# Optimization experiments

Hardware: AMD Instinct MI355X
Metric: run time of the kernel (lower is better)

Reference implementation:

```python
import jax, jax.numpy as jnp
import numpy as np

B, P, IN_DIM, OUT_DIM = 4, 120000, 4, 64
SPATIAL = (480, 360, 32)
EPS = 1e-5
SLOPE = 0.01  # LeakyReLU default negative slope


def setup_inputs() -> dict:
    key = jax.random.key(0)
    ks = jax.random.split(key, 10)
    pc = jax.random.normal(ks[0], (B, P, IN_DIM), dtype=jnp.float32)
    pc_indices = jax.random.randint(ks[1], (B, P, 3), 0, 32, dtype=jnp.int32)
    W1 = jax.random.normal(ks[2], (IN_DIM, 16), dtype=jnp.float32) * (1.0 / np.sqrt(IN_DIM))
    b1 = jax.random.normal(ks[3], (16,), dtype=jnp.float32) * 0.01
    g1 = jnp.ones((16,), jnp.float32)
    be1 = jnp.zeros((16,), jnp.float32)
    W2 = jax.random.normal(ks[4], (16, OUT_DIM), dtype=jnp.float32) * 0.25
    b2 = jax.random.normal(ks[5], (OUT_DIM,), dtype=jnp.float32) * 0.01
    g2 = jnp.ones((OUT_DIM,), jnp.float32)
    be2 = jnp.zeros((OUT_DIM,), jnp.float32)
    return {"pc": pc, "pc_indices": pc_indices, "W1": W1, "b1": b1, "g1": g1,
            "be1": be1, "W2": W2, "b2": b2, "g2": g2, "be2": be2}


def _bn_lrelu(h, g, b):
    # BatchNorm1d in training mode: batch mean / biased variance over points
    mean = jnp.mean(h, axis=0)
    var = jnp.mean((h - mean) ** 2, axis=0)
    h = (h - mean) / jnp.sqrt(var + EPS) * g + b
    return jnp.where(h >= 0, h, SLOPE * h)


def reference(pc, pc_indices, W1, b1, g1, be1, W2, b2, g2, be2):
    N = B * P
    x = pc.reshape(N, IN_DIM)
    bid = jnp.repeat(jnp.arange(B, dtype=jnp.int32), P)  # batch id padded in front
    coords = jnp.concatenate([bid[:, None], pc_indices.reshape(N, 3)], axis=1)  # [N,4]

    # small MLP (shuffle/recover in the original is a mathematical no-op for outputs)
    h = _bn_lrelu(x @ W1 + b1, g1, be1)
    feat = _bn_lrelu(h @ W2 + b2, g2, be2)  # [N, OUT_DIM]

    # torch.unique(dim=0) == lexicographic sort of linearized voxel keys
    S0, S1, S2 = SPATIAL
    key = (((coords[:, 0] * S0 + coords[:, 1]) * S1 + coords[:, 2]) * S2 + coords[:, 3])
    order = jnp.argsort(key)
    sk = key[order]
    is_first = jnp.concatenate([jnp.ones((1,), bool), sk[1:] != sk[:-1]])
    seg_sorted = (jnp.cumsum(is_first) - 1).astype(jnp.int32)  # segment id per sorted point
    inv = jnp.zeros((N,), jnp.int32).at[order].set(seg_sorted)  # inverse index (unsorted)

    # scatter_max into (padded, fixed-shape) voxel feature table
    voxel_feat = jax.ops.segment_max(feat, inv, num_segments=N)  # [N, OUT_DIM]
    n_uni = seg_sorted[-1] + 1
    valid = jnp.arange(N) < n_uni
    voxel_feat = jnp.where(valid[:, None], voxel_feat, 0.0)
    voxel_ind = jnp.zeros((N, 4), jnp.int32).at[seg_sorted].set(coords[order])

    return voxel_feat, voxel_ind, feat
```

## Files before the change

### kernel.cpp

```cpp
#include <hip/hip_runtime.h>

typedef unsigned int u32;
typedef unsigned long long u64;

#define N_PTS 480000
#define PPB   120000
#define NKEY  131072
#define NBLK_A 256
#define NBLK_B 256
#define SLOPE 0.01f

__global__ __launch_bounds__(256) void kA0(const float* __restrict__ pc,
                                           const int* __restrict__ pidx,
                                           u32* __restrict__ keys,
                                           u32* __restrict__ cnt,
                                           float* __restrict__ pA) {
    int t = threadIdx.x;
    int g = blockIdx.x * 256 + t;
    ((u64*)cnt)[g] = 0ull;

    float a[14];
#pragma unroll
    for (int j = 0; j < 14; ++j) a[j] = 0.f;

    for (int n = g; n < N_PTS; n += NBLK_A * 256) {
        float4 x = ((const float4*)pc)[n];
        a[0] += x.x; a[1] += x.y; a[2] += x.z; a[3] += x.w;
        a[4] += x.x * x.x; a[5] += x.x * x.y; a[6]  += x.x * x.z; a[7]  += x.x * x.w;
        a[8] += x.y * x.y; a[9] += x.y * x.z; a[10] += x.y * x.w;
        a[11] += x.z * x.z; a[12] += x.z * x.w; a[13] += x.w * x.w;

        int i0 = pidx[3 * n], i1 = pidx[3 * n + 1], i2 = pidx[3 * n + 2];
        int bid = n / PPB;
        keys[n] = (u32)(bid * 32768 + i0 * 1024 + i1 * 32 + i2);
    }

    __shared__ float red[256];
    for (int j = 0; j < 14; ++j) {
        red[t] = a[j];
        __syncthreads();
        for (int s = 128; s > 0; s >>= 1) {
            if (t < s) red[t] += red[t + s];
            __syncthreads();
        }
        if (t == 0) pA[j * NBLK_A + blockIdx.x] = red[0];
        __syncthreads();
    }
}

__global__ __launch_bounds__(256, 1) void kB(const float* __restrict__ pc,
                                             const u32* __restrict__ keys,
                                             const float* __restrict__ pA,
                                             const float* __restrict__ W1,
                                             const float* __restrict__ b1,
                                             const float* __restrict__ g1,
                                             const float* __restrict__ be1,
                                             u32* __restrict__ cnt,
                                             float* __restrict__ pB,
                                             float* __restrict__ stats1) {
    int t = threadIdx.x, w = t >> 6, lane = t & 63;
    __shared__ float S[14];
    __shared__ float sW[80];
    __shared__ float sred[4][152];

    for (int q = w; q < 14; q += 4) {
        const float* p = pA + q * NBLK_A;
        float s = p[lane] + p[lane + 64] + p[lane + 128] + p[lane + 192];
        for (int d = 32; d > 0; d >>= 1) s += __shfl_xor(s, d);
        if (lane == 0) S[q] = s;
    }
    __syncthreads();
    if (t < 16) {
        int c = t;
        double w4[4];
#pragma unroll
        for (int i = 0; i < 4; ++i) w4[i] = W1[i * 16 + c];
        double sx[4] = { S[0], S[1], S[2], S[3] };
        auto sxx = [&](int i, int j) -> double {
            if (i > j) { int k = i; i = j; j = k; }
            int base = (i == 0) ? 4 : (i == 1) ? 8 : (i == 2) ? 11 : 13;
            return (double)S[base + (j - i)];
        };
        double su = 0.0;
        for (int i = 0; i < 4; ++i) su += sx[i] * w4[i];
        double q = 0.0;
        for (int i = 0; i < 4; ++i)
            for (int j = 0; j < 4; ++j) q += w4[i] * w4[j] * sxx(i, j);
        double b = (double)b1[c];
        double sum   = su + b * (double)N_PTS;
        double sumsq = q + 2.0 * b * su + (double)N_PTS * b * b;
        double mean = sum / (double)N_PTS;
        double var  = sumsq / (double)N_PTS - mean * mean;
        float inv = rsqrtf((float)(var + 1e-5));
        float sc = g1[c] * inv;
        float sf = be1[c] - (float)mean * sc;
#pragma unroll
        for (int i = 0; i < 4; ++i) sW[c * 4 + i] = W1[i * 16 + c] * sc;
        sW[64 + c] = b1[c] * sc + sf;
        if (blockIdx.x == 0) {
#pragma unroll
            for (int i = 0; i < 4; ++i) stats1[c * 4 + i] = sW[c * 4 + i];
            stats1[64 + c] = sW[64 + c];
        }
    }
    __syncthreads();

    for (int n = blockIdx.x * 256 + t; n < N_PTS; n += NBLK_B * 256)
        atomicAdd(&cnt[keys[n]], 1u);

    float acc[152];
#pragma unroll
    for (int m = 0; m < 152; ++m) acc[m] = 0.f;

    const float4* sW4 = (const float4*)sW;
    for (int n = blockIdx.x * 256 + t; n < N_PTS; n += NBLK_B * 256) {
        float4 x = ((const float4*)pc)[n];
        float h[16];
#pragma unroll
        for (int k = 0; k < 16; ++k) {
            float4 wk = sW4[k];
            float z = x.x * wk.x + x.y * wk.y + x.z * wk.z + x.w * wk.w + sW[64 + k];
            h[k] = (z >= 0.f) ? z : SLOPE * z;
        }
#pragma unroll
        for (int i = 0; i < 16; ++i) acc[i] += h[i];
#pragma unroll
        for (int i = 0; i < 16; ++i)
#pragma unroll
            for (int j = i; j < 16; ++j)
                acc[16 + i * 16 - (i * (i - 1)) / 2 + (j - i)] += h[i] * h[j];
    }

#pragma unroll
    for (int m = 0; m < 152; ++m) {
        float s = acc[m];
        for (int d = 32; d > 0; d >>= 1) s += __shfl_xor(s, d);
        acc[m] = s;
    }
    if (lane == 0) {
#pragma unroll
        for (int m = 0; m < 152; ++m) sred[w][m] = acc[m];
    }
    __syncthreads();
    if (t < 152)
        pB[t * NBLK_B + blockIdx.x] = sred[0][t] + sred[1][t] + sred[2][t] + sred[3][t];
}

__global__ __launch_bounds__(256) void kS1(const u32* __restrict__ cnt,
                                           u32* __restrict__ bsum,
                                           const float* __restrict__ pB,
                                           const float* __restrict__ W2,
                                           const float* __restrict__ b2,
                                           const float* __restrict__ g2,
                                           const float* __restrict__ be2,
                                           float* __restrict__ stats2) {
    int t = threadIdx.x, b = blockIdx.x;
    uint4 c4 = ((const uint4*)cnt)[b * 256 + t];
    u32 cs = c4.x + c4.y + c4.z + c4.w;
    u32 os = (c4.x > 0) + (c4.y > 0) + (c4.z > 0) + (c4.w > 0);
    __shared__ u32 rc[256], ro[256];
    rc[t] = cs; ro[t] = os;
    __syncthreads();
    for (int s = 128; s > 0; s >>= 1) {
        if (t < s) { rc[t] += rc[t + s]; ro[t] += ro[t + s]; }
        __syncthreads();
    }
    if (t == 0) { bsum[2 * b] = rc[0]; bsum[2 * b + 1] = ro[0]; }

    if (b == 0) {
        int w = t >> 6, lane = t & 63;
        __shared__ float S[152];
        for (int q = w; q < 152; q += 4) {
            const float* p = pB + q * NBLK_B;
            float s = p[lane] + p[lane + 64] + p[lane + 128] + p[lane + 192];
            for (int d = 32; d > 0; d >>= 1) s += __shfl_xor(s, d);
            if (lane == 0) S[q] = s;
        }
        __syncthreads();
        if (t < 64) {
            double wv[16];
#pragma unroll
            for (int k = 0; k < 16; ++k) wv[k] = W2[k * 64 + t];
            double sh = 0.0;
            for (int k = 0; k < 16; ++k) sh += wv[k] * (double)S[k];
            auto qidx = [&](int i, int j) { return 16 + i * 16 - (i * (i - 1)) / 2 + (j - i); };
            double q = 0.0;
            for (int i = 0; i < 16; ++i) {
                q += wv[i] * wv[i] * (double)S[qidx(i, i)];
                double t2 = 0.0;
                for (int j = i + 1; j < 16; ++j) t2 += wv[j] * (double)S[qidx(i, j)];
                q += 2.0 * wv[i] * t2;
            }
            double bb = (double)b2[t];
            double sum   = sh + bb * (double)N_PTS;
            double sumsq = q + 2.0 * bb * sh + (double)N_PTS * bb * bb;
            double mean = sum / (double)N_PTS;
            double var  = sumsq / (double)N_PTS - mean * mean;
            float inv = rsqrtf((float)(var + 1e-5));
            float scs = g2[t] * inv;
            float sf = be2[t] - (float)mean * scs;
#pragma unroll
            for (int k = 0; k < 16; ++k) stats2[k * 64 + t] = W2[k * 64 + t] * scs;
            stats2[1024 + t] = b2[t] * scs + sf;
        }
    }
}

__global__ __launch_bounds__(256) void kS2(u32* __restrict__ cnt,
                                           const u32* __restrict__ bsum,
                                           u32* __restrict__ startc,
                                           float* __restrict__ vi,
                                           u32* __restrict__ nuni) {
    int t = threadIdx.x, b = blockIdx.x;
    __shared__ u32 sbc[128], sbo[128];
    __shared__ u32 cOff, oOff;
    __shared__ u64 scan[256];
    if (t < 128) { sbc[t] = bsum[2 * t]; sbo[t] = bsum[2 * t + 1]; }

    uint4 c4 = ((const uint4*)cnt)[b * 256 + t];
    u32 cv[4] = { c4.x, c4.y, c4.z, c4.w };
    u32 cs = cv[0] + cv[1] + cv[2] + cv[3];
    u32 os = (cv[0] > 0) + (cv[1] > 0) + (cv[2] > 0) + (cv[3] > 0);
    scan[t] = ((u64)cs << 32) | (u64)os;
    __syncthreads();
    if (t == 0) {
        u32 a = 0, o = 0;
        for (int i = 0; i < b; ++i) { a += sbc[i]; o += sbo[i]; }
        cOff = a; oOff = o;
    }
    for (int d = 1; d < 256; d <<= 1) {
        u64 v = (t >= d) ? scan[t - d] : 0ull;
        __syncthreads();
        scan[t] += v;
        __syncthreads();
    }
    u64 ex = scan[t] - (((u64)cs << 32) | (u64)os);
    u32 start = cOff + (u32)(ex >> 32);
    u32 rank  = oOff + (u32)(ex & 0xffffffffull);

    int kbase = b * 1024 + t * 4;
#pragma unroll
    for (int j = 0; j < 4; ++j) {
        u32 k = (u32)(kbase + j);
        cnt[k] = start;
        if (cv[j] > 0) {
            startc[rank] = start;
            float4 o;
            o.x = (float)(k >> 15);
            o.y = (float)((k >> 10) & 31);
            o.z = (float)((k >> 5) & 31);
            o.w = (float)(k & 31);
            ((float4*)vi)[rank] = o;
            rank++;
        }
        start += cv[j];
    }
    if (b == 127 && t == 255) {
        nuni[0] = rank;
        startc[rank] = N_PTS;
    }
}

__global__ __launch_bounds__(256) void kP(const u32* __restrict__ keys,
                                          u32* __restrict__ cursor,
                                          u32* __restrict__ pid) {
    int n = blockIdx.x * 256 + threadIdx.x;
    if (n < N_PTS) {
        u32 k = keys[n];
        u32 pos = atomicAdd(&cursor[k], 1u);
        pid[pos] = (u32)n;
    }
}

__global__ __launch_bounds__(256) void kW(const float* __restrict__ pc,
                                          const u32* __restrict__ pid,
                                          const u32* __restrict__ startc,
                                          const u32* __restrict__ nuni,
                                          const float* __restrict__ stats1,
                                          const float* __restrict__ stats2,
                                          float* __restrict__ feat,
                                          float* __restrict__ vf,
                                          float* __restrict__ vi) {
    u32 nu = *nuni;
    int w = threadIdx.x >> 6, lane = threadIdx.x & 63;

    int k1 = lane & 15;
    float w1c[4];
#pragma unroll
    for (int i = 0; i < 4; ++i) w1c[i] = stats1[k1 * 4 + i];
    float c1 = stats1[64 + k1];

    float w2c[16];
#pragma unroll
    for (int k = 0; k < 16; ++k) w2c[k] = stats2[k * 64 + lane];
    float c2f = stats2[1024 + lane];

    for (u32 r = blockIdx.x * 4 + (u32)w; r < N_PTS; r += 8192) {
        if (r < nu) {
            u32 s = startc[r], e = startc[r + 1];
            float m = -3.4e38f;
            for (u32 i = s; i < e; ++i) {
                u32 p = pid[i];
                float4 x = ((const float4*)pc)[p];
                float hk = x.x * w1c[0] + x.y * w1c[1] + x.z * w1c[2] + x.w * w1c[3] + c1;
                hk = (hk >= 0.f) ? hk : SLOPE * hk;
                u32 hbits = __float_as_uint(hk);
                float f = c2f;
#pragma unroll
                for (int k = 0; k < 16; ++k) {
                    float hv = __uint_as_float((u32)__builtin_amdgcn_readlane((int)hbits, k));
                    f += hv * w2c[k];
                }
                f = (f >= 0.f) ? f : SLOPE * f;
                feat[(size_t)p * 64 + lane] = f;
                m = fmaxf(m, f);
            }
            vf[(size_t)r * 64 + lane] = m;
        } else {
            vf[(size_t)r * 64 + lane] = 0.f;
            if (lane < 4) vi[(size_t)r * 4 + lane] = 0.f;
        }
    }
}

extern "C" void kernel_launch(void* const* d_in, const int* in_sizes, int n_in,
                              void* d_out, int out_size, void* d_ws, size_t ws_size,
                              hipStream_t stream) {
    const float* pc   = (const float*)d_in[0];
    const int*   pidx = (const int*)d_in[1];
    const float* W1   = (const float*)d_in[2];
    const float* b1   = (const float*)d_in[3];
    const float* g1   = (const float*)d_in[4];
    const float* be1  = (const float*)d_in[5];
    const float* W2   = (const float*)d_in[6];
    const float* b2   = (const float*)d_in[7];
    const float* g2   = (const float*)d_in[8];
    const float* be2  = (const float*)d_in[9];

    float* vf   = (float*)d_out;
    float* vi   = vf + (size_t)N_PTS * 64;
    float* feat = vi + (size_t)N_PTS * 4;

    u32* ws     = (u32*)d_ws;
    u32* keys   = ws;
    u32* cnt    = ws + 480000;
    u32* startc = ws + 611072;
    u32* bsum   = ws + 742148;
    u32* nuni   = ws + 742404;
    u32* pid    = ws + 742420;
    float* pA     = (float*)(ws + 1222420);
    float* stats1 = (float*)(ws + 1226004);
    float* pB     = (float*)(ws + 1226084);
    float* stats2 = (float*)(ws + 1264996);

    kA0<<<NBLK_A, 256, 0, stream>>>(pc, pidx, keys, cnt, pA);
    kB<<<NBLK_B, 256, 0, stream>>>(pc, keys, pA, W1, b1, g1, be1, cnt, pB, stats1);
    kS1<<<128, 256, 0, stream>>>(cnt, bsum, pB, W2, b2, g2, be2, stats2);
    kS2<<<128, 256, 0, stream>>>(cnt, bsum, startc, vi, nuni);
    kP<<<1875, 256, 0, stream>>>(keys, cnt, pid);
    kW<<<2048, 256, 0, stream>>>(pc, pid, startc, nuni, stats1, stats2, feat, vf, vi);
}
```

Measured before the change: 191.3 us.

## Write per-point features coalesced in scatter kernel, give voxel kernel contiguous row ranges

Moves the per-point feature computation and store into the scatter kernel (kP becomes kC), where each wave writes 64 consecutive points' features in order, so the writes are coalesced instead of landing at gathered point ids. The voxel max kernel no longer stores feat and now handles a contiguous chunk of 64 voxel rows per wave rather than a grid stride. Waves whose whole chunk lies beyond the unique count return early after zero-filling with float4 stores. The cost is running the point MLP twice, once in kC and again in kW for the max.

Result: slower. 343.8 us (+79.7%).

```diff
diff --git a/kernel.cpp b/kernel.cpp
--- a/kernel.cpp
+++ b/kernel.cpp
@@ -261,14 +261,46 @@
     }
 }
 
-__global__ __launch_bounds__(256) void kP(const u32* __restrict__ keys,
+__global__ __launch_bounds__(256) void kC(const float* __restrict__ pc,
+                                          const u32* __restrict__ keys,
                                           u32* __restrict__ cursor,
-                                          u32* __restrict__ pid) {
-    int n = blockIdx.x * 256 + threadIdx.x;
-    if (n < N_PTS) {
-        u32 k = keys[n];
+                                          u32* __restrict__ pid,
+                                          const float* __restrict__ stats1,
+                                          const float* __restrict__ stats2,
+                                          float* __restrict__ feat) {
+    int t = threadIdx.x;
+    int n0 = blockIdx.x * 256 + t;
+    {
+        u32 k = keys[n0];
         u32 pos = atomicAdd(&cursor[k], 1u);
-        pid[pos] = (u32)n;
+        pid[pos] = (u32)n0;
+    }
+
+    int w = t >> 6, lane = t & 63;
+    int k1 = lane & 15;
+    float w1c[4];
+#pragma unroll
+    for (int i = 0; i < 4; ++i) w1c[i] = stats1[k1 * 4 + i];
+    float c1 = stats1[64 + k1];
+    float w2c[16];
+#pragma unroll
+    for (int k = 0; k < 16; ++k) w2c[k] = stats2[k * 64 + lane];
+    float c2f = stats2[1024 + lane];
+
+    u32 p0 = (u32)(blockIdx.x * 4 + w) * 64;
+    for (u32 p = p0; p < p0 + 64; ++p) {
+        float4 x = ((const float4*)pc)[p];
+        float hk = x.x * w1c[0] + x.y * w1c[1] + x.z * w1c[2] + x.w * w1c[3] + c1;
+        hk = (hk >= 0.f) ? hk : SLOPE * hk;
+        u32 hbits = __float_as_uint(hk);
+        float f = c2f;
+#pragma unroll
+        for (int k = 0; k < 16; ++k) {
+            float hv = __uint_as_float((u32)__builtin_amdgcn_readlane((int)hbits, k));
+            f += hv * w2c[k];
+        }
+        f = (f >= 0.f) ? f : SLOPE * f;
+        feat[(size_t)p * 64 + lane] = f;
     }
 }
 
@@ -278,24 +310,32 @@
                                           const u32* __restrict__ nuni,
                                           const float* __restrict__ stats1,
                                           const float* __restrict__ stats2,
-                                          float* __restrict__ feat,
                                           float* __restrict__ vf,
                                           float* __restrict__ vi) {
     u32 nu = *nuni;
-    int w = threadIdx.x >> 6, lane = threadIdx.x & 63;
+    int t = threadIdx.x, w = t >> 6, lane = t & 63;
+    u32 r0 = (u32)(blockIdx.x * 4 + w) * 64;
+
+    if (r0 >= nu) {
+        float4 z; z.x = 0.f; z.y = 0.f; z.z = 0.f; z.w = 0.f;
+        float4* dst = (float4*)(vf + (size_t)r0 * 64);
+#pragma unroll
+        for (int i = 0; i < 16; ++i) dst[i * 64 + lane] = z;
+        ((float4*)(vi + (size_t)r0 * 4))[lane] = z;
+        return;
+    }
 
     int k1 = lane & 15;
     float w1c[4];
 #pragma unroll
     for (int i = 0; i < 4; ++i) w1c[i] = stats1[k1 * 4 + i];
     float c1 = stats1[64 + k1];
-
     float w2c[16];
 #pragma unroll
     for (int k = 0; k < 16; ++k) w2c[k] = stats2[k * 64 + lane];
     float c2f = stats2[1024 + lane];
 
-    for (u32 r = blockIdx.x * 4 + (u32)w; r < N_PTS; r += 8192) {
+    for (u32 r = r0; r < r0 + 64; ++r) {
         if (r < nu) {
             u32 s = startc[r], e = startc[r + 1];
             float m = -3.4e38f;
@@ -312,7 +352,6 @@
                     f += hv * w2c[k];
                 }
                 f = (f >= 0.f) ? f : SLOPE * f;
-                feat[(size_t)p * 64 + lane] = f;
                 m = fmaxf(m, f);
             }
             vf[(size_t)r * 64 + lane] = m;
@@ -357,6 +396,6 @@
     kB<<<NBLK_B, 256, 0, stream>>>(pc, keys, pA, W1, b1, g1, be1, cnt, pB, stats1);
     kS1<<<128, 256, 0, stream>>>(cnt, bsum, pB, W2, b2, g2, be2, stats2);
     kS2<<<128, 256, 0, stream>>>(cnt, bsum, startc, vi, nuni);
-    kP<<<1875, 256, 0, stream>>>(keys, cnt, pid);
-    kW<<<2048, 256, 0, stream>>>(pc, pid, startc, nuni, stats1, stats2, feat, vf, vi);
-}
+    kC<<<1875, 256, 0, stream>>>(pc, keys, cnt, pid, stats1, stats2, feat);
+    kW<<<1875, 256, 0, stream>>>(pc, pid, startc, nuni, stats1, stats2, vf, vi);
+}
```
